# Performance work log

Measured on AMD Instinct MI355X. Metric: run time of the kernel, lower is better.

## Reference

```python
import jax, jax.numpy as jnp
import numpy as np

EMB = 64
N_LEFT = 100000   # m: rows of left_features, b
N_RIGHT = 100000  # n: rows of right_features, c
N_EDGES = 3200000


def setup_inputs() -> dict:
    key = jax.random.key(0)
    ks = jax.random.split(key, 12)
    inp = {
        "left_features": jax.random.normal(ks[0], (N_LEFT, EMB), jnp.float32),
        "right_features_k": jax.random.normal(ks[1], (N_RIGHT, EMB), jnp.float32),
        "edge_index": jax.random.randint(ks[2], (N_EDGES, 2), 0, N_RIGHT, jnp.int64),
        "edge_weight": jax.random.uniform(ks[3], (N_EDGES,), jnp.float32),
        "right_features": jax.random.normal(ks[4], (N_RIGHT, EMB), jnp.float32),
        "c": jax.random.normal(ks[5], (N_RIGHT, 1), jnp.float32),
        "b": jax.random.normal(ks[6], (N_LEFT, 1), jnp.float32),
        # learned parameters
        "temp": jnp.full((2,), 0.9, jnp.float32),
        "W1": jax.random.normal(ks[7], (EMB, EMB), jnp.float32) * 0.05,
        "b1": jnp.zeros((EMB,), jnp.float32),
        "W2": jax.random.normal(ks[8], (EMB, EMB), jnp.float32) * 0.05,
        "b2": jnp.zeros((EMB,), jnp.float32),
    }
    return inp


def reference(left_features, right_features_k, edge_index, edge_weight,
              right_features, c, b, temp, W1, b1, W2, b2):
    # right_to_left=False branch of BipartiteGraphConvolution.forward
    n = right_features.shape[0]  # = c.shape[0]
    # Source quirk: values.sum(dim=-1) on a 1-D vector is a GLOBAL scalar sum,
    # clamped to min 1; every edge weight is scaled by 1/that scalar.
    total = jnp.maximum(jnp.sum(edge_weight), 1.0)
    vals = edge_weight / total                                    # [E]
    row = edge_index[:, 0]  # destination (right) node, in [0, n)
    col = edge_index[:, 1]  # source (left) node, in [0, m)
    # sparse-dense matmul: conv_output = A @ left_features, A in COO (coalesce
    # just sums duplicate entries, identical to segment-sum over raw edges)
    msg = left_features[col] * vals[:, None]                      # [E, EMB]
    conv_output = jax.ops.segment_sum(msg, row, num_segments=n)   # [n, EMB]
    h = right_features + temp[1] * (c - conv_output)              # [n, EMB]
    # output_module: Linear -> ReLU -> Linear (torch Linear: x @ W.T + b)
    h = jax.nn.relu(h @ W1.T + b1)
    out = h @ W2.T + b2
    return out
```

## Files before the change

kernel.cpp:

```cpp
#include <hip/hip_runtime.h>

#define EMB 64
#define BROWS 512
#define BSHIFT 9
#define CHUNK 4096
#define COLBITS 23
#define COLMASK ((1u << COLBITS) - 1u)
#define MROWS 64
#define HPAD 66

__device__ __forceinline__ unsigned short f2bf(float f) {
    unsigned u = __float_as_uint(f);
    u = u + 0x7FFFu + ((u >> 16) & 1u);
    return (unsigned short)(u >> 16);
}

__global__ void convert_left_kernel(const float* __restrict__ left,
                                    unsigned* __restrict__ left16, int n2) {
    int i = blockIdx.x * blockDim.x + threadIdx.x;
    if (i >= n2) return;
    float2 v = ((const float2*)left)[i];
    left16[i] = (unsigned)f2bf(v.x) | ((unsigned)f2bf(v.y) << 16);
}

__global__ void init_bcur_kernel(int* __restrict__ bcur, int nb, int slot) {
    int t = threadIdx.x;
    if (t < nb) bcur[t] = t * slot;
}

__global__ __launch_bounds__(256) void partition_kernel(
    const int2* __restrict__ eidx, const float* __restrict__ w, int n_edges,
    int* __restrict__ bcursor, int2* __restrict__ bsorted,
    float* __restrict__ total) {
    __shared__ int lh[256];
    __shared__ int lo[256];
    __shared__ int go[256];
    __shared__ int lcur[256];
    __shared__ int2 stage[CHUNK];
    __shared__ int dstg[CHUNK];
    int t = threadIdx.x;
    int base = blockIdx.x * CHUNK;
    int cnt = min(CHUNK, n_edges - base);

    lh[t] = 0;
    __syncthreads();
    #pragma unroll
    for (int k = 0; k < CHUNK / 256; ++k) {
        int e = base + t + k * 256;
        if (e < n_edges) atomicAdd(&lh[eidx[e].x >> BSHIFT], 1);
    }
    __syncthreads();
    int v = lh[t];
    lo[t] = v;
    __syncthreads();
    for (int off = 1; off < 256; off <<= 1) {
        int u = (t >= off) ? lo[t - off] : 0;
        __syncthreads();
        lo[t] += u;
        __syncthreads();
    }
    int excl = lo[t] - v;
    go[t] = (v > 0) ? atomicAdd(&bcursor[t], v) : 0;
    __syncthreads();
    lo[t] = excl;
    lcur[t] = excl;
    __syncthreads();

    float s = 0.f;
    #pragma unroll
    for (int k = 0; k < CHUNK / 256; ++k) {
        int e = base + t + k * 256;
        if (e < n_edges) {
            int2 rc = eidx[e];
            float wv = w[e];
            s += wv;
            int b = rc.x >> BSHIFT;
            unsigned rl = (unsigned)(rc.x & (BROWS - 1));
            int p = atomicAdd(&lcur[b], 1);
            stage[p] = make_int2((int)((rl << COLBITS) | (unsigned)rc.y),
                                 __float_as_int(wv));
            dstg[p] = go[b] + (p - lo[b]);
        }
    }
    #pragma unroll
    for (int off = 32; off > 0; off >>= 1) s += __shfl_down(s, off, 64);
    if ((t & 63) == 0) atomicAdd(total, s);
    __syncthreads();
    #pragma unroll
    for (int k = 0; k < CHUNK / 256; ++k) {
        int s2 = t + k * 256;
        if (s2 < cnt) bsorted[dstg[s2]] = stage[s2];
    }
}

__global__ __launch_bounds__(256, 1) void count_scan_kernel(
    const int* __restrict__ bcur, int* __restrict__ sbase, int nb, int slot) {
    __shared__ int ssc[256];
    int t = threadIdx.x;
    int cnt = (t < nb) ? (bcur[t] - t * slot) : 0;
    ssc[t] = cnt;
    __syncthreads();
    for (int off = 1; off < 256; off <<= 1) {
        int u = (t >= off) ? ssc[t - off] : 0;
        __syncthreads();
        ssc[t] += u;
        __syncthreads();
    }
    if (t < nb) sbase[t] = ssc[t] - cnt;
}

__global__ __launch_bounds__(256) void local_rowsort_kernel(
    const int2* __restrict__ bsorted, const int* __restrict__ bcur,
    const int* __restrict__ sbase, int* __restrict__ offs,
    int2* __restrict__ sorted2, int n_right, int slot) {
    __shared__ int lhist[BROWS];
    __shared__ int lcur[BROWS];
    __shared__ int ps[256];
    int b = blockIdx.x;
    int t = threadIdx.x;
    int src0 = b * slot;
    int send = min(bcur[b], src0 + slot);
    int dbase = sbase[b];
    int row0 = b << BSHIFT;
    int nrows = min(BROWS, n_right - row0);

    lhist[2 * t] = 0;
    lhist[2 * t + 1] = 0;
    __syncthreads();
    for (int e = src0 + t; e < send; e += 256)
        atomicAdd(&lhist[((unsigned)bsorted[e].x) >> COLBITS], 1);
    __syncthreads();

    int v0 = lhist[2 * t];
    int v1 = lhist[2 * t + 1];
    int pv = v0 + v1;
    ps[t] = pv;
    __syncthreads();
    for (int off = 1; off < 256; off <<= 1) {
        int u = (t >= off) ? ps[t - off] : 0;
        __syncthreads();
        ps[t] += u;
        __syncthreads();
    }
    int epair = ps[t] - pv;
    lcur[2 * t] = epair;
    lcur[2 * t + 1] = epair + v0;
    if (2 * t < nrows)     offs[row0 + 2 * t]     = dbase + epair;
    if (2 * t + 1 < nrows) offs[row0 + 2 * t + 1] = dbase + epair + v0;
    __syncthreads();

    int e = src0 + t;
    for (; e + 3 * 256 < send; e += 4 * 256) {
        int2 e0 = bsorted[e + 0 * 256];
        int2 e1 = bsorted[e + 1 * 256];
        int2 e2 = bsorted[e + 2 * 256];
        int2 e3 = bsorted[e + 3 * 256];
        int p0 = atomicAdd(&lcur[((unsigned)e0.x) >> COLBITS], 1);
        int p1 = atomicAdd(&lcur[((unsigned)e1.x) >> COLBITS], 1);
        int p2 = atomicAdd(&lcur[((unsigned)e2.x) >> COLBITS], 1);
        int p3 = atomicAdd(&lcur[((unsigned)e3.x) >> COLBITS], 1);
        sorted2[dbase + p0] = e0;
        sorted2[dbase + p1] = e1;
        sorted2[dbase + p2] = e2;
        sorted2[dbase + p3] = e3;
    }
    for (; e < send; e += 256) {
        int2 e0 = bsorted[e];
        int p0 = atomicAdd(&lcur[((unsigned)e0.x) >> COLBITS], 1);
        sorted2[dbase + p0] = e0;
    }
}

__global__ void seg_gather_bf16_kernel(const int2* __restrict__ sorted,
                                       const int* __restrict__ offs,
                                       const uint4* __restrict__ left16o,
                                       const float* __restrict__ right,
                                       const float* __restrict__ c,
                                       const float* __restrict__ temp,
                                       const float* __restrict__ total,
                                       float* __restrict__ hout, int n_right,
                                       int n_edges, int offs_are_ends) {
    int gid = blockIdx.x * blockDim.x + threadIdx.x;
    int wid = gid >> 6;
    int lane = gid & 63;
    if (wid >= n_right) return;
    int start, end;
    if (offs_are_ends) {
        end = offs[wid];
        start = (wid == 0) ? 0 : offs[wid - 1];
    } else {
        start = offs[wid];
        end = (wid + 1 < n_right) ? offs[wid + 1] : n_edges;
    }

    int sub = lane >> 3;
    int d8  = lane & 7;

    float cv = c[wid];
    float inv = 1.0f / fmaxf(total[0], 1.0f);
    float t1 = temp[1];

    float a0 = 0.f, a1 = 0.f, a2 = 0.f, a3 = 0.f;
    float a4 = 0.f, a5 = 0.f, a6 = 0.f, a7 = 0.f;

    if (start < end) {
        int ee = start + sub;
        int2 sv = sorted[(ee < end) ? ee : (end - 1)];
        for (int base = start; base < end; base += 8) {
            int2 cur = sv;
            int ecur = base + sub;
            int bnext = base + 8;
            if (bnext < end) {
                int en = bnext + sub;
                sv = sorted[(en < end) ? en : (end - 1)];
            }
            float wv = (ecur < end) ? __int_as_float(cur.y) : 0.f;
            unsigned col = (unsigned)cur.x & COLMASK;
            uint4 pk = left16o[(size_t)col * 8 + d8];
            a0 = fmaf(wv, __uint_as_float(pk.x << 16), a0);
            a1 = fmaf(wv, __uint_as_float(pk.x & 0xffff0000u), a1);
            a2 = fmaf(wv, __uint_as_float(pk.y << 16), a2);
            a3 = fmaf(wv, __uint_as_float(pk.y & 0xffff0000u), a3);
            a4 = fmaf(wv, __uint_as_float(pk.z << 16), a4);
            a5 = fmaf(wv, __uint_as_float(pk.z & 0xffff0000u), a5);
            a6 = fmaf(wv, __uint_as_float(pk.w << 16), a6);
            a7 = fmaf(wv, __uint_as_float(pk.w & 0xffff0000u), a7);
        }
    }

    #define RED8(x) x += __shfl_xor(x, 8, 64); x += __shfl_xor(x, 16, 64); \
                    x += __shfl_xor(x, 32, 64);
    RED8(a0) RED8(a1) RED8(a2) RED8(a3) RED8(a4) RED8(a5) RED8(a6) RED8(a7)
    #undef RED8

    if (lane < 8) {
        const float4* rp = (const float4*)(right + (size_t)wid * EMB);
        float4 r0 = rp[2 * lane];
        float4 r1 = rp[2 * lane + 1];
        float4 h0, h1;
        h0.x = r0.x + t1 * (cv - a0 * inv);
        h0.y = r0.y + t1 * (cv - a1 * inv);
        h0.z = r0.z + t1 * (cv - a2 * inv);
        h0.w = r0.w + t1 * (cv - a3 * inv);
        h1.x = r1.x + t1 * (cv - a4 * inv);
        h1.y = r1.y + t1 * (cv - a5 * inv);
        h1.z = r1.z + t1 * (cv - a6 * inv);
        h1.w = r1.w + t1 * (cv - a7 * inv);
        float4* op = (float4*)(hout + (size_t)wid * EMB);
        op[2 * lane] = h0;
        op[2 * lane + 1] = h1;
    }
}

__global__ __launch_bounds__(256, 4) void mlp_kernel(
    const float* __restrict__ W1, const float* __restrict__ b1,
    const float* __restrict__ W2, const float* __restrict__ b2,
    float* __restrict__ io, int n) {
    __shared__ float hT[64 * HPAD];
    __shared__ float h1T[64 * 64];
    int t = threadIdx.x;
    int r = t & 63;
    int q = __builtin_amdgcn_readfirstlane(t >> 6);
    int row0 = blockIdx.x * MROWS;

    #pragma unroll
    for (int i = 0; i < 16; ++i) {
        int rr = i * 4 + q;
        int gr = row0 + rr;
        float v = (gr < n) ? io[(size_t)gr * EMB + r] : 0.f;
        hT[r * HPAD + rr] = v;
    }
    __syncthreads();

    float acc[16];
    #pragma unroll
    for (int jj = 0; jj < 16; ++jj) acc[jj] = b1[q * 16 + jj];
    for (int k = 0; k < 64; ++k) {
        float hk = hT[k * HPAD + r];
        #pragma unroll
        for (int jj = 0; jj < 16; ++jj)
            acc[jj] = fmaf(hk, W1[(q * 16 + jj) * EMB + k], acc[jj]);
    }
    #pragma unroll
    for (int jj = 0; jj < 16; ++jj)
        h1T[(q * 16 + jj) * 64 + r] = fmaxf(acc[jj], 0.f);
    __syncthreads();

    #pragma unroll
    for (int jj = 0; jj < 16; ++jj) acc[jj] = b2[q * 16 + jj];
    for (int k = 0; k < 64; ++k) {
        float hk = h1T[k * 64 + r];
        #pragma unroll
        for (int jj = 0; jj < 16; ++jj)
            acc[jj] = fmaf(hk, W2[(q * 16 + jj) * EMB + k], acc[jj]);
    }
    __syncthreads();
    #pragma unroll
    for (int jj = 0; jj < 16; ++jj)
        hT[(q * 16 + jj) * HPAD + r] = acc[jj];
    __syncthreads();

    #pragma unroll
    for (int i = 0; i < 16; ++i) {
        int rr = i * 4 + q;
        int gr = row0 + rr;
        if (gr < n) io[(size_t)gr * EMB + r] = hT[r * HPAD + rr];
    }
}


__global__ void hist_total_kernel(const int2* __restrict__ eidx,
                                  const float* __restrict__ w, int n_edges,
                                  int* __restrict__ counts,
                                  float* __restrict__ total) {
    int gid = blockIdx.x * blockDim.x + threadIdx.x;
    int stride = gridDim.x * blockDim.x;
    float s = 0.f;
    for (int e = gid; e < n_edges; e += stride) {
        s += w[e];
        atomicAdd(&counts[eidx[e].x], 1);
    }
    #pragma unroll
    for (int off = 32; off > 0; off >>= 1) s += __shfl_down(s, off, 64);
    if ((threadIdx.x & 63) == 0) atomicAdd(total, s);
}

__global__ __launch_bounds__(1024, 1) void scan1_kernel(
    const int* __restrict__ cnt, int* __restrict__ incl,
    int* __restrict__ bsums, int n) {
    __shared__ int s[1024];
    int t = threadIdx.x;
    int i = blockIdx.x * 1024 + t;
    int v = (i < n) ? cnt[i] : 0;
    s[t] = v;
    __syncthreads();
    for (int off = 1; off < 1024; off <<= 1) {
        int u = (t >= off) ? s[t - off] : 0;
        __syncthreads();
        s[t] += u;
        __syncthreads();
    }
    if (i < n) incl[i] = s[t];
    if (t == 1023) bsums[blockIdx.x] = s[t];
}

__global__ __launch_bounds__(256, 1) void scan2_kernel(int* __restrict__ bsums, int nb) {
    __shared__ int s[256];
    int t = threadIdx.x;
    int v = (t < nb) ? bsums[t] : 0;
    s[t] = v;
    __syncthreads();
    for (int off = 1; off < 256; off <<= 1) {
        int u = (t >= off) ? s[t - off] : 0;
        __syncthreads();
        s[t] += u;
        __syncthreads();
    }
    if (t < nb) bsums[t] = s[t] - v;
}

__global__ void scan3_kernel(const int* __restrict__ incl,
                             const int* __restrict__ base,
                             int* __restrict__ offs, int n) {
    int i = blockIdx.x * blockDim.x + threadIdx.x;
    if (i >= n) return;
    offs[i] = (i == 0) ? 0 : incl[i - 1] + base[(i - 1) >> 10];
}

__global__ void scatter_kernel(const int2* __restrict__ eidx,
                               const float* __restrict__ w, int n_edges,
                               int* __restrict__ offs,
                               int2* __restrict__ sorted) {
    int gid = blockIdx.x * blockDim.x + threadIdx.x;
    int stride = gridDim.x * blockDim.x;
    for (int e = gid; e < n_edges; e += stride) {
        int2 rc = eidx[e];
        float v = w[e];
        int pos = atomicAdd(&offs[rc.x], 1);
        sorted[pos] = make_int2(rc.y, __float_as_int(v));
    }
}


__global__ void sum_weights_kernel(const float* __restrict__ w, int n,
                                   float* __restrict__ total) {
    int gid = blockIdx.x * blockDim.x + threadIdx.x;
    int stride = gridDim.x * blockDim.x;
    float s = 0.f;
    for (int i = gid; i < n; i += stride) s += w[i];
    #pragma unroll
    for (int off = 32; off > 0; off >>= 1) s += __shfl_down(s, off, 64);
    if ((threadIdx.x & 63) == 0) atomicAdd(total, s);
}

__global__ void edge_scatter_kernel(const int* __restrict__ idx,
                                    const float* __restrict__ w,
                                    const float* __restrict__ left,
                                    const float* __restrict__ total,
                                    float* __restrict__ conv,
                                    long long n_threads) {
    long long gid = (long long)blockIdx.x * blockDim.x + threadIdx.x;
    if (gid >= n_threads) return;
    int e = (int)(gid >> 6);
    int d = (int)(gid & 63);
    float inv = 1.0f / fmaxf(total[0], 1.0f);
    int row = idx[2 * e];
    int col = idx[2 * e + 1];
    float v = w[e] * inv;
    float msg = left[(size_t)col * EMB + d] * v;
    atomicAdd(&conv[(size_t)row * EMB + d], msg);
}

__global__ __launch_bounds__(256, 1) void fused_mlp_kernel(
    const float* __restrict__ right, const float* __restrict__ c,
    const float* __restrict__ temp,
    const float* __restrict__ W1, const float* __restrict__ b1,
    const float* __restrict__ W2, const float* __restrict__ b2,
    float* __restrict__ io, int n) {
    int r = blockIdx.x * blockDim.x + threadIdx.x;
    if (r >= n) return;
    float t1 = temp[1];
    float cv = c[r];
    float h[EMB];
    const float4* rp = (const float4*)(right + (size_t)r * EMB);
    const float4* qp = (const float4*)(io + (size_t)r * EMB);
    #pragma unroll
    for (int qq = 0; qq < EMB / 4; ++qq) {
        float4 rv = rp[qq];
        float4 qv = qp[qq];
        h[4 * qq + 0] = rv.x + t1 * (cv - qv.x);
        h[4 * qq + 1] = rv.y + t1 * (cv - qv.y);
        h[4 * qq + 2] = rv.z + t1 * (cv - qv.z);
        h[4 * qq + 3] = rv.w + t1 * (cv - qv.w);
    }
    float h1[EMB];
    #pragma unroll
    for (int j = 0; j < EMB; j += 4) {
        float s0 = b1[j], s1 = b1[j + 1], s2 = b1[j + 2], s3 = b1[j + 3];
        #pragma unroll
        for (int k = 0; k < EMB; ++k) {
            float hk = h[k];
            s0 = fmaf(hk, W1[(j + 0) * EMB + k], s0);
            s1 = fmaf(hk, W1[(j + 1) * EMB + k], s1);
            s2 = fmaf(hk, W1[(j + 2) * EMB + k], s2);
            s3 = fmaf(hk, W1[(j + 3) * EMB + k], s3);
        }
        h1[j] = fmaxf(s0, 0.f);
        h1[j + 1] = fmaxf(s1, 0.f);
        h1[j + 2] = fmaxf(s2, 0.f);
        h1[j + 3] = fmaxf(s3, 0.f);
    }
    float4* op = (float4*)(io + (size_t)r * EMB);
    #pragma unroll
    for (int j = 0; j < EMB; j += 4) {
        float s0 = b2[j], s1 = b2[j + 1], s2 = b2[j + 2], s3 = b2[j + 3];
        #pragma unroll
        for (int k = 0; k < EMB; ++k) {
            float hk = h1[k];
            s0 = fmaf(hk, W2[(j + 0) * EMB + k], s0);
            s1 = fmaf(hk, W2[(j + 1) * EMB + k], s1);
            s2 = fmaf(hk, W2[(j + 2) * EMB + k], s2);
            s3 = fmaf(hk, W2[(j + 3) * EMB + k], s3);
        }
        op[j / 4] = make_float4(s0, s1, s2, s3);
    }
}


extern "C" void kernel_launch(void* const* d_in, const int* in_sizes, int n_in,
                              void* d_out, int out_size, void* d_ws, size_t ws_size,
                              hipStream_t stream) {
    const float* left   = (const float*)d_in[0];
    const int*   eidx   = (const int*)d_in[2];
    const float* ew     = (const float*)d_in[3];
    const float* right  = (const float*)d_in[4];
    const float* c      = (const float*)d_in[5];
    const float* temp   = (const float*)d_in[7];
    const float* W1     = (const float*)d_in[8];
    const float* b1     = (const float*)d_in[9];
    const float* W2     = (const float*)d_in[10];
    const float* b2     = (const float*)d_in[11];

    const int n_edges = in_sizes[3];
    const int n_right = in_sizes[4] / EMB;
    const int n_left  = in_sizes[0] / EMB;
    float* out = (float*)d_out;

    const int nb = (n_right + BROWS - 1) >> BSHIFT;
    const int nblocks_scan = (n_right + 1023) / 1024;

    auto align256 = [](size_t x) { return (x + 255) & ~(size_t)255; };

    int slot = n_edges / (nb > 0 ? nb : 1);
    slot += slot / 16 + 128;

    size_t off_bcur    = 64;
    size_t off_sbase   = align256(off_bcur + (size_t)nb * 4);
    size_t off_offs    = align256(off_sbase + (size_t)(nb + 1) * 4);
    size_t off_bsorted = align256(off_offs + (size_t)n_right * 4);
    size_t off_sorted2 = align256(off_bsorted + ((size_t)nb * slot + slot) * 8);
    size_t off_left16f = align256(off_sorted2 + (size_t)n_edges * 8);
    size_t req_full    = off_left16f + (size_t)n_left * EMB * 2;

    size_t m_off_offs   = 64;
    size_t m_off_incl   = align256(m_off_offs + (size_t)n_right * 4);
    size_t m_off_bsum   = align256(m_off_incl + (size_t)n_right * 4);
    size_t m_off_sorted = align256(m_off_bsum + 1024);
    size_t m_off_left16 = align256(m_off_sorted + (size_t)n_edges * 8);
    size_t req_mid      = m_off_left16 + (size_t)n_left * EMB * 2;

    bool common_ok = (nb <= 256) && (nblocks_scan <= 256) &&
                     (n_left <= (1 << COLBITS)) && (BROWS * nb >= n_right);

    if (common_ok && ws_size >= req_full) {
        char* ws = (char*)d_ws;
        float* total = (float*)ws;
        int* bcur = (int*)(ws + off_bcur);
        int* sbase = (int*)(ws + off_sbase);
        int* offs = (int*)(ws + off_offs);
        int2* bsorted = (int2*)(ws + off_bsorted);
        int2* sorted2 = (int2*)(ws + off_sorted2);
        unsigned short* left16 = (unsigned short*)(ws + off_left16f);

        hipMemsetAsync(ws, 0, 64, stream);

        int n2 = n_left * EMB / 2;
        convert_left_kernel<<<(n2 + 255) / 256, 256, 0, stream>>>(
            left, (unsigned*)left16, n2);
        init_bcur_kernel<<<1, 256, 0, stream>>>(bcur, nb, slot);
        {
            int nchunks = (n_edges + CHUNK - 1) / CHUNK;
            partition_kernel<<<nchunks, 256, 0, stream>>>(
                (const int2*)eidx, ew, n_edges, bcur, bsorted, total);
        }
        count_scan_kernel<<<1, 256, 0, stream>>>(bcur, sbase, nb, slot);
        local_rowsort_kernel<<<nb, 256, 0, stream>>>(bsorted, bcur, sbase, offs,
                                                     sorted2, n_right, slot);
        {
            long long n_threads = (long long)n_right * EMB;
            int blocks = (int)((n_threads + 255) / 256);
            seg_gather_bf16_kernel<<<blocks, 256, 0, stream>>>(
                sorted2, offs, (const uint4*)left16, right, c, temp, total,
                out, n_right, n_edges, 0);
        }
        mlp_kernel<<<(n_right + MROWS - 1) / MROWS, 256, 0, stream>>>(
            W1, b1, W2, b2, out, n_right);
    } else if (common_ok && ws_size >= req_mid) {
        char* ws = (char*)d_ws;
        float* total = (float*)ws;
        int* offs = (int*)(ws + m_off_offs);
        int* incl = (int*)(ws + m_off_incl);
        int* bsum = (int*)(ws + m_off_bsum);
        int2* sorted = (int2*)(ws + m_off_sorted);
        unsigned short* left16 = (unsigned short*)(ws + m_off_left16);

        hipMemsetAsync(ws, 0, m_off_offs + (size_t)n_right * 4, stream);

        int n2 = n_left * EMB / 2;
        convert_left_kernel<<<(n2 + 255) / 256, 256, 0, stream>>>(
            left, (unsigned*)left16, n2);
        hist_total_kernel<<<2048, 256, 0, stream>>>((const int2*)eidx, ew,
                                                    n_edges, offs, total);
        scan1_kernel<<<nblocks_scan, 1024, 0, stream>>>(offs, incl, bsum, n_right);
        scan2_kernel<<<1, 256, 0, stream>>>(bsum, nblocks_scan);
        scan3_kernel<<<(n_right + 255) / 256, 256, 0, stream>>>(incl, bsum, offs,
                                                                n_right);
        scatter_kernel<<<2048, 256, 0, stream>>>((const int2*)eidx, ew, n_edges,
                                                 offs, sorted);
        {
            long long n_threads = (long long)n_right * EMB;
            int blocks = (int)((n_threads + 255) / 256);
            seg_gather_bf16_kernel<<<blocks, 256, 0, stream>>>(
                sorted, offs, (const uint4*)left16, right, c, temp, total,
                out, n_right, n_edges, 1);
        }
        mlp_kernel<<<(n_right + MROWS - 1) / MROWS, 256, 0, stream>>>(
            W1, b1, W2, b2, out, n_right);
    } else {
        float* total = (float*)d_ws;
        hipMemsetAsync(d_out, 0, (size_t)out_size * sizeof(float), stream);
        hipMemsetAsync(d_ws, 0, sizeof(float), stream);
        sum_weights_kernel<<<2048, 256, 0, stream>>>(ew, n_edges, total);
        long long n_threads = (long long)n_edges * EMB;
        long long blocks = (n_threads + 255) / 256;
        edge_scatter_kernel<<<(int)blocks, 256, 0, stream>>>(
            eidx, ew, left, total, out, n_threads);
        int mblocks = (n_right + 255) / 256;
        fused_mlp_kernel<<<mblocks, 256, 0, stream>>>(right, c, temp, W1, b1, W2,
                                                      b2, out, n_right);
    }
}
```

Before: 255.4 us.

## Simplify bucket partition to register-held single-pass scatter; widen row-sort blocks

The partition kernel drops the separate histogram pass, prefix scan and shared-memory staging. Each thread keeps its 8 edges in registers, takes local ranks with shared atomics, reserves global bucket space once per block, then scatters directly. Chunks shrink to 2048 edges, so more blocks launch and per-block global atomics double. The local row sort now runs 1024 threads per bucket, one thread per row, which adds parallelism per block but makes the 512-entry scan serial over more threads; the unstaged scatter is also less coalesced.

```diff
diff --git a/kernel.cpp b/kernel.cpp
--- a/kernel.cpp
+++ b/kernel.cpp
@@ -3,7 +3,7 @@
 #define EMB 64
 #define BROWS 512
 #define BSHIFT 9
-#define CHUNK 4096
+#define CHUNK2 2048
 #define COLBITS 23
 #define COLMASK ((1u << COLBITS) - 1u)
 #define MROWS 64
@@ -28,68 +28,54 @@
     if (t < nb) bcur[t] = t * slot;
 }
 
-__global__ __launch_bounds__(256) void partition_kernel(
+__global__ __launch_bounds__(256) void partition2_kernel(
     const int2* __restrict__ eidx, const float* __restrict__ w, int n_edges,
-    int* __restrict__ bcursor, int2* __restrict__ bsorted,
+    int nb, int* __restrict__ bcursor, int2* __restrict__ bsorted,
     float* __restrict__ total) {
-    __shared__ int lh[256];
-    __shared__ int lo[256];
+    __shared__ int lcur[256];
     __shared__ int go[256];
-    __shared__ int lcur[256];
-    __shared__ int2 stage[CHUNK];
-    __shared__ int dstg[CHUNK];
-    int t = threadIdx.x;
-    int base = blockIdx.x * CHUNK;
-    int cnt = min(CHUNK, n_edges - base);
-
-    lh[t] = 0;
-    __syncthreads();
-    #pragma unroll
-    for (int k = 0; k < CHUNK / 256; ++k) {
-        int e = base + t + k * 256;
-        if (e < n_edges) atomicAdd(&lh[eidx[e].x >> BSHIFT], 1);
-    }
-    __syncthreads();
-    int v = lh[t];
-    lo[t] = v;
-    __syncthreads();
-    for (int off = 1; off < 256; off <<= 1) {
-        int u = (t >= off) ? lo[t - off] : 0;
-        __syncthreads();
-        lo[t] += u;
-        __syncthreads();
-    }
-    int excl = lo[t] - v;
-    go[t] = (v > 0) ? atomicAdd(&bcursor[t], v) : 0;
-    __syncthreads();
-    lo[t] = excl;
-    lcur[t] = excl;
-    __syncthreads();
-
+    int t = threadIdx.x;
+    int base = blockIdx.x * CHUNK2;
+
+    lcur[t] = 0;
+    __syncthreads();
+
+    int2 pay[8];
+    int bb[8];
+    int rr[8];
     float s = 0.f;
     #pragma unroll
-    for (int k = 0; k < CHUNK / 256; ++k) {
+    for (int k = 0; k < 8; ++k) {
         int e = base + t + k * 256;
         if (e < n_edges) {
             int2 rc = eidx[e];
             float wv = w[e];
             s += wv;
             int b = rc.x >> BSHIFT;
-            unsigned rl = (unsigned)(rc.x & (BROWS - 1));
-            int p = atomicAdd(&lcur[b], 1);
-            stage[p] = make_int2((int)((rl << COLBITS) | (unsigned)rc.y),
-                                 __float_as_int(wv));
-            dstg[p] = go[b] + (p - lo[b]);
+            pay[k] = make_int2(
+                (int)(((unsigned)(rc.x & (BROWS - 1)) << COLBITS) |
+                      (unsigned)rc.y),
+                __float_as_int(wv));
+            bb[k] = b;
+            rr[k] = atomicAdd(&lcur[b], 1);
+        } else {
+            bb[k] = -1;
         }
     }
     #pragma unroll
     for (int off = 32; off > 0; off >>= 1) s += __shfl_down(s, off, 64);
     if ((t & 63) == 0) atomicAdd(total, s);
     __syncthreads();
-    #pragma unroll
-    for (int k = 0; k < CHUNK / 256; ++k) {
-        int s2 = t + k * 256;
-        if (s2 < cnt) bsorted[dstg[s2]] = stage[s2];
+
+    if (t < nb) {
+        int v = lcur[t];
+        go[t] = (v > 0) ? atomicAdd(&bcursor[t], v) : 0;
+    }
+    __syncthreads();
+
+    #pragma unroll
+    for (int k = 0; k < 8; ++k) {
+        if (bb[k] >= 0) bsorted[(size_t)go[bb[k]] + rr[k]] = pay[k];
     }
 }
 
@@ -109,13 +95,13 @@
     if (t < nb) sbase[t] = ssc[t] - cnt;
 }
 
-__global__ __launch_bounds__(256) void local_rowsort_kernel(
+__global__ __launch_bounds__(1024) void local_rowsort_kernel(
     const int2* __restrict__ bsorted, const int* __restrict__ bcur,
     const int* __restrict__ sbase, int* __restrict__ offs,
     int2* __restrict__ sorted2, int n_right, int slot) {
     __shared__ int lhist[BROWS];
     __shared__ int lcur[BROWS];
-    __shared__ int ps[256];
+    __shared__ int ps[BROWS];
     int b = blockIdx.x;
     int t = threadIdx.x;
     int src0 = b * slot;
@@ -124,37 +110,33 @@
     int row0 = b << BSHIFT;
     int nrows = min(BROWS, n_right - row0);
 
-    lhist[2 * t] = 0;
-    lhist[2 * t + 1] = 0;
-    __syncthreads();
-    for (int e = src0 + t; e < send; e += 256)
+    if (t < BROWS) lhist[t] = 0;
+    __syncthreads();
+    for (int e = src0 + t; e < send; e += 1024)
         atomicAdd(&lhist[((unsigned)bsorted[e].x) >> COLBITS], 1);
     __syncthreads();
 
-    int v0 = lhist[2 * t];
-    int v1 = lhist[2 * t + 1];
-    int pv = v0 + v1;
-    ps[t] = pv;
-    __syncthreads();
-    for (int off = 1; off < 256; off <<= 1) {
-        int u = (t >= off) ? ps[t - off] : 0;
-        __syncthreads();
-        ps[t] += u;
-        __syncthreads();
-    }
-    int epair = ps[t] - pv;
-    lcur[2 * t] = epair;
-    lcur[2 * t + 1] = epair + v0;
-    if (2 * t < nrows)     offs[row0 + 2 * t]     = dbase + epair;
-    if (2 * t + 1 < nrows) offs[row0 + 2 * t + 1] = dbase + epair + v0;
+    if (t < BROWS) ps[t] = lhist[t];
+    __syncthreads();
+    for (int off = 1; off < BROWS; off <<= 1) {
+        int u = (t < BROWS && t >= off) ? ps[t - off] : 0;
+        __syncthreads();
+        if (t < BROWS) ps[t] += u;
+        __syncthreads();
+    }
+    if (t < BROWS) {
+        int excl = ps[t] - lhist[t];
+        lcur[t] = excl;
+        if (t < nrows) offs[row0 + t] = dbase + excl;
+    }
     __syncthreads();
 
     int e = src0 + t;
-    for (; e + 3 * 256 < send; e += 4 * 256) {
-        int2 e0 = bsorted[e + 0 * 256];
-        int2 e1 = bsorted[e + 1 * 256];
-        int2 e2 = bsorted[e + 2 * 256];
-        int2 e3 = bsorted[e + 3 * 256];
+    for (; e + 3 * 1024 < send; e += 4 * 1024) {
+        int2 e0 = bsorted[e + 0 * 1024];
+        int2 e1 = bsorted[e + 1 * 1024];
+        int2 e2 = bsorted[e + 2 * 1024];
+        int2 e3 = bsorted[e + 3 * 1024];
         int p0 = atomicAdd(&lcur[((unsigned)e0.x) >> COLBITS], 1);
         int p1 = atomicAdd(&lcur[((unsigned)e1.x) >> COLBITS], 1);
         int p2 = atomicAdd(&lcur[((unsigned)e2.x) >> COLBITS], 1);
@@ -164,7 +146,7 @@
         sorted2[dbase + p2] = e2;
         sorted2[dbase + p3] = e3;
     }
-    for (; e < send; e += 256) {
+    for (; e < send; e += 1024) {
         int2 e0 = bsorted[e];
         int p0 = atomicAdd(&lcur[((unsigned)e0.x) >> COLBITS], 1);
         sorted2[dbase + p0] = e0;
@@ -529,13 +511,13 @@
             left, (unsigned*)left16, n2);
         init_bcur_kernel<<<1, 256, 0, stream>>>(bcur, nb, slot);
         {
-            int nchunks = (n_edges + CHUNK - 1) / CHUNK;
-            partition_kernel<<<nchunks, 256, 0, stream>>>(
-                (const int2*)eidx, ew, n_edges, bcur, bsorted, total);
+            int nchunks = (n_edges + CHUNK2 - 1) / CHUNK2;
+            partition2_kernel<<<nchunks, 256, 0, stream>>>(
+                (const int2*)eidx, ew, n_edges, nb, bcur, bsorted, total);
         }
         count_scan_kernel<<<1, 256, 0, stream>>>(bcur, sbase, nb, slot);
-        local_rowsort_kernel<<<nb, 256, 0, stream>>>(bsorted, bcur, sbase, offs,
-                                                     sorted2, n_right, slot);
+        local_rowsort_kernel<<<nb, 1024, 0, stream>>>(bsorted, bcur, sbase, offs,
+                                                      sorted2, n_right, slot);
         {
             long long n_threads = (long long)n_right * EMB;
             int blocks = (int)((n_threads + 255) / 256);
```

After: 271.7 us. 6.4% more time.
